# Kernel optimization log

Measured on AMD Instinct MI355X. Metric: run time of the kernel, lower is better.

## Reference

```python
import jax, jax.numpy as jnp
import numpy as np

C = 1024
R = 4            # reduction
A = 10           # num_adapters
LN_EPS = 1e-5
THRESHOLDS = np.array([1/9, 1/7, 1/5, 1/3, 1.0, 3.0, 5.0, 7.0, 9.0], dtype=np.float32)


def setup_inputs() -> dict:
    key = jax.random.key(0)
    k_feat, k_ar, k_w1, k_w2 = jax.random.split(key, 4)
    B, NA, H, W = 2, 3, 64, 64
    Cr = C // R
    output_feat = jax.random.normal(k_feat, (B, C, H, W), jnp.float32)
    # aspect ratios in [0,10) so all 10 adapters get selected
    aspect_ratio = jax.random.uniform(k_ar, (B, NA, H, W), jnp.float32) * 10.0
    # LayerNorm params (torch default init: weight=1, bias=0), stacked over adapters
    ln_scale = jnp.ones((A, C), jnp.float32)
    ln_bias = jnp.zeros((A, C), jnp.float32)
    # kaiming_normal_ fan_out / relu: std = sqrt(2/fan_out); torch weight [out,in]
    # w1 here is [C, Cr] == torch weight [Cr, C].T, fan_out = Cr
    w1 = jax.random.normal(k_w1, (A, C, Cr), jnp.float32) * np.sqrt(2.0 / Cr)
    # w2 here is [Cr, C] == torch weight [C, Cr].T, fan_out = C
    w2 = jax.random.normal(k_w2, (A, Cr, C), jnp.float32) * np.sqrt(2.0 / C)
    return dict(output_feat=output_feat, aspect_ratio=aspect_ratio,
                ln_scale=ln_scale, ln_bias=ln_bias, w1=w1, w2=w2)


def reference(output_feat, aspect_ratio, ln_scale, ln_bias, w1, w2):
    B, Cc, H, W = output_feat.shape
    NA = aspect_ratio.shape[1]
    HW = H * W
    # tokens [N, C]
    x = output_feat.transpose(0, 2, 3, 1).reshape(-1, Cc)
    # shared LayerNorm normalization (per-adapter affine applied after)
    mu = jnp.mean(x, axis=-1, keepdims=True)
    var = jnp.var(x, axis=-1, keepdims=True)
    norm = (x - mu) * jax.lax.rsqrt(var + LN_EPS)              # [N, C]
    y = norm[None, :, :] * ln_scale[:, None, :] + ln_bias[:, None, :]  # [A, N, C]
    h = jax.nn.gelu(jnp.einsum('anc,acd->and', y, w1), approximate=False)
    adapter_out = jnp.einsum('and,adc->anc', h, w2)            # [A, N, C]
    adapter_out = adapter_out.reshape(A, B, HW, Cc)            # [A, B, HW, C]
    # per-anchor, per-pixel adapter index from aspect ratio vs thresholds
    thr = jnp.asarray(THRESHOLDS, dtype=aspect_ratio.dtype)
    ar = aspect_ratio.reshape(B, NA, HW)
    idx = jnp.sum(ar[..., None] > thr, axis=-1)                # [B, NA, HW] in [0, 9]
    # gather selected adapter output per (batch, anchor, pixel)
    b_idx = jnp.arange(B)[:, None, None]
    p_idx = jnp.arange(HW)[None, None, :]
    selected = adapter_out[idx, b_idx, p_idx]                  # [B, NA, HW, C]
    selected = selected.mean(axis=1).reshape(B, H, W, Cc).transpose(0, 3, 1, 2)
    return selected + output_feat
```

## Files before the change

kernel.cpp:

```cpp
#include <hip/hip_runtime.h>
#include <hip/hip_bf16.h>
#include <math.h>

#define C_DIM 1024
#define CR    256
#define A_N   10
#define NANCH 3
#define B_N   2
#define HW_N  4096
#define NTOK  (B_N*HW_N)
#define KG2   (A_N*CR)

typedef unsigned short ushort_t;
typedef __attribute__((ext_vector_type(4))) float f32x4;
typedef __attribute__((ext_vector_type(8))) short bf16x8;

__device__ __forceinline__ ushort_t f2bf(float x) {
    __hip_bfloat16 h = __float2bfloat16(x);
    return *reinterpret_cast<ushort_t*>(&h);
}
__device__ __forceinline__ float bf2f(ushort_t u) {
    return __uint_as_float(((unsigned)u) << 16);
}

__device__ __forceinline__ float fast_gelu(float x) {
    float t = x * x;
    float u = x * (-1.5957691216f - 0.0713548163f * t);
    float e = __expf(u);
    return x * __frcp_rn(1.0f + e);
}

__global__ __launch_bounds__(256) void prep_all(
    const float* __restrict__ w1, const float* __restrict__ w2,
    const float* __restrict__ ln_s, const float* __restrict__ ln_b,
    const float* __restrict__ feat, const float* __restrict__ ar,
    ushort_t* __restrict__ w1t, ushort_t* __restrict__ w2t,
    float* __restrict__ bias1, float* __restrict__ sumv, float* __restrict__ sumq,
    int* __restrict__ cnt, int* __restrict__ tokw, int* __restrict__ tokmap) {
    __shared__ float lds[64][65];
    __shared__ float bb[4][64];
    __shared__ int lcnt[A_N], lpos[A_N], gbase[A_N];
    int id = blockIdx.x, tid = threadIdx.x;
    int lo = tid & 63, hi = tid >> 6;

    if (id < 640) {
        int d0 = (id & 3) * 64, c0 = ((id >> 2) & 15) * 64, a = id >> 6;
        #pragma unroll
        for (int i = 0; i < 16; i++) {
            int c_l = i * 4 + hi;
            lds[c_l][lo] = w1[((size_t)a * C_DIM + c0 + c_l) * CR + d0 + lo];
        }
        __syncthreads();
        {
            float s = 0.f;
            #pragma unroll
            for (int cc = 0; cc < 16; cc++) {
                int c = hi * 16 + cc;
                s += lds[c][lo] * ln_b[a * C_DIM + c0 + c];
            }
            bb[hi][lo] = s;
        }
        float sc = ln_s[a * C_DIM + c0 + lo];
        #pragma unroll
        for (int i = 0; i < 16; i++) {
            int d_l = i * 4 + hi;
            w1t[((size_t)a * CR + d0 + d_l) * C_DIM + c0 + lo] = f2bf(lds[lo][d_l] * sc);
        }
        __syncthreads();
        if (hi == 0)
            atomicAdd(&bias1[a * CR + d0 + lo], bb[0][lo] + bb[1][lo] + bb[2][lo] + bb[3][lo]);
    } else if (id < 1280) {
        int id2 = id - 640;
        int k0 = (id2 % 40) * 64, c0 = (id2 / 40) * 64;
        #pragma unroll
        for (int i = 0; i < 16; i++) {
            int k_l = i * 4 + hi;
            lds[k_l][lo] = w2[((size_t)k0 + k_l) * C_DIM + c0 + lo];
        }
        __syncthreads();
        #pragma unroll
        for (int i = 0; i < 16; i++) {
            int c_l = i * 4 + hi;
            w2t[((size_t)c0 + c_l) * KG2 + k0 + lo] = f2bf(lds[lo][c_l]);
        }
    } else if (id < 2304) {
        int id2 = id - 1280;
        int p0 = (id2 & 63) * 64, c0 = ((id2 >> 6) & 7) * 128, b = id2 >> 9;
        int p = lo, cs = hi;
        float s = 0.f, s2 = 0.f;
        #pragma unroll
        for (int c = cs; c < 128; c += 4) {
            float v = feat[((size_t)b * C_DIM + c0 + c) * HW_N + p0 + p];
            s += v; s2 += v * v;
        }
        float (*sh)[64] = (float(*)[64])lds;
        sh[cs][p] = s; sh[cs + 4][p] = s2;
        __syncthreads();
        if (tid < 64) {
            float ss = sh[0][tid] + sh[1][tid] + sh[2][tid] + sh[3][tid];
            float qq = sh[4][tid] + sh[5][tid] + sh[6][tid] + sh[7][tid];
            int t = b * HW_N + p0 + tid;
            atomicAdd(&sumv[t], ss);
            atomicAdd(&sumq[t], qq);
        }
    } else {
        if (tid < A_N) { lcnt[tid] = 0; lpos[tid] = 0; }
        __syncthreads();
        int t = (id - 2304) * 256 + tid;
        int b = t >> 12, p = t & (HW_N - 1);
        const float THR[9] = {1.0f/9.0f, 1.0f/7.0f, 0.2f, 1.0f/3.0f, 1.0f, 3.0f, 5.0f, 7.0f, 9.0f};
        int idxs[NANCH];
        #pragma unroll
        for (int na = 0; na < NANCH; na++) {
            float v = ar[(size_t)b * NANCH * HW_N + na * HW_N + p];
            int idx = 0;
            #pragma unroll
            for (int i = 0; i < 9; i++) idx += (v > THR[i]) ? 1 : 0;
            idxs[na] = idx;
        }
        int myA[NANCH], myC[NANCH], nmine = 0;
        #pragma unroll
        for (int j = 0; j < NANCH; j++) {
            bool first = true; int c3 = 0;
            #pragma unroll
            for (int k = 0; k < NANCH; k++) {
                if (idxs[k] == idxs[j]) { c3++; if (k < j) first = false; }
            }
            if (first) {
                myA[nmine] = idxs[j];
                myC[nmine] = c3;
                nmine++;
                atomicAdd(&lcnt[idxs[j]], 1);
            }
        }
        __syncthreads();
        if (tid < A_N) gbase[tid] = atomicAdd(&cnt[tid], lcnt[tid]);
        __syncthreads();
        for (int i = 0; i < NANCH; i++) {
            if (i < nmine) {
                int a2 = myA[i];
                int slot = atomicAdd(&lpos[a2], 1);
                int pos = gbase[a2] + slot;
                tokw[a2 * NTOK + pos] = t;
                tokmap[t * 3 + i] = pos | (a2 << 13) | (myC[i] << 17);
            } else {
                tokmap[t * 3 + i] = 0;
            }
        }
    }
}

__global__ __launch_bounds__(256) void normk(const float* __restrict__ feat,
                                             const float* __restrict__ sumv,
                                             const float* __restrict__ sumq,
                                             ushort_t* __restrict__ normG) {
    int p0 = blockIdx.x * 64, c0 = blockIdx.y * 64, b = blockIdx.z;
    __shared__ float lds[64][65];
    int tid = threadIdx.x, lo = tid & 63, hi = tid >> 6;
    #pragma unroll
    for (int i = 0; i < 16; i++) {
        int c_l = i * 4 + hi;
        lds[c_l][lo] = feat[((size_t)b * C_DIM + c0 + c_l) * HW_N + p0 + lo];
    }
    __syncthreads();
    int t_l = tid >> 3, cg = tid & 7;
    #pragma unroll
    for (int ii = 0; ii < 2; ii++) {
        int tl = ii * 32 + t_l;
        int t = b * HW_N + p0 + tl;
        float m = sumv[t] * (1.f / C_DIM);
        float q = sumq[t] * (1.f / C_DIM);
        float r = rsqrtf(q - m * m + 1e-5f);
        bf16x8 v;
        #pragma unroll
        for (int k = 0; k < 8; k++)
            v[k] = (short)f2bf((lds[cg * 8 + k][tl] - m) * r);
        *(bf16x8*)(normG + (size_t)t * C_DIM + c0 + cg * 8) = v;
    }
}

__device__ __forceinline__ void gemm_core_ptrs(
    const ushort_t* const ap[4], const ushort_t* const bp[4],
    int K, ushort_t* As, ushort_t* Bs, f32x4 acc[4][4]) {
    const int tid = threadIdx.x;
    const int lane = tid & 63;
    const int w = tid >> 6;
    const int wr = w >> 1, wc = w & 1;
    const int lrow = lane & 15;
    const int quad = lane >> 4;
    const int swzr = lrow & 7;

    #pragma unroll
    for (int i = 0; i < 4; i++)
        #pragma unroll
        for (int j = 0; j < 4; j++)
            #pragma unroll
            for (int e = 0; e < 4; e++) acc[i][j][e] = 0.f;

    for (int k0 = 0; k0 < K; k0 += 64) {
        __syncthreads();
        #pragma unroll
        for (int i = 0; i < 4; i++) {
            __builtin_amdgcn_global_load_lds(
                (__attribute__((address_space(1))) void*)(ap[i] + k0),
                (__attribute__((address_space(3))) void*)(As + (w * 32 + i * 8) * 64),
                16, 0, 0);
            __builtin_amdgcn_global_load_lds(
                (__attribute__((address_space(1))) void*)(bp[i] + k0),
                (__attribute__((address_space(3))) void*)(Bs + (w * 32 + i * 8) * 64),
                16, 0, 0);
        }
        __syncthreads();
        #pragma unroll
        for (int ks = 0; ks < 2; ks++) {
            const int cidx = ((ks * 4 + quad) ^ swzr) * 8;
            bf16x8 af[4], bfr[4];
            #pragma unroll
            for (int mt = 0; mt < 4; mt++)
                af[mt] = *(const bf16x8*)(As + (wr * 64 + mt * 16 + lrow) * 64 + cidx);
            #pragma unroll
            for (int nt = 0; nt < 4; nt++)
                bfr[nt] = *(const bf16x8*)(Bs + (wc * 64 + nt * 16 + lrow) * 64 + cidx);
            #pragma unroll
            for (int mt = 0; mt < 4; mt++)
                #pragma unroll
                for (int nt = 0; nt < 4; nt++)
                    acc[mt][nt] = __builtin_amdgcn_mfma_f32_16x16x32_bf16(af[mt], bfr[nt], acc[mt][nt], 0, 0, 0);
        }
    }
}

__global__ __launch_bounds__(256) void gemm1c(const ushort_t* __restrict__ normG,
                                              const ushort_t* __restrict__ w1t,
                                              const float* __restrict__ bias1,
                                              const int* __restrict__ tokw,
                                              const int* __restrict__ cnt,
                                              ushort_t* __restrict__ Hc) {
    int a = blockIdx.z;
    int mcount = cnt[a];
    int m0 = blockIdx.y * 128;
    if (m0 >= mcount) return;
    int n0 = blockIdx.x * 128;
    int base = 0;
    for (int a2 = 0; a2 < a; a2++) base += cnt[a2];

    __shared__ __align__(16) ushort_t As[128 * 64];
    __shared__ __align__(16) ushort_t Bs[128 * 64];

    int tid = threadIdx.x, lane = tid & 63, w = tid >> 6;
    int lrow8 = lane >> 3;
    int scol = ((lane & 7) ^ lrow8) * 8;
    int srowl = w * 32 + lrow8;

    const ushort_t* ap[4];
    const ushort_t* bp[4];
    #pragma unroll
    for (int i = 0; i < 4; i++) {
        int rt = tokw[a * NTOK + m0 + srowl + i * 8] & (NTOK - 1);
        ap[i] = normG + (size_t)rt * C_DIM + scol;
        bp[i] = w1t + ((size_t)a * CR + n0 + srowl + i * 8) * C_DIM + scol;
    }

    f32x4 acc[4][4];
    gemm_core_ptrs(ap, bp, C_DIM, As, Bs, acc);

    int wr = w >> 1, wc = w & 1, lrow = lane & 15, quad = lane >> 4;
    float bi[4];
    #pragma unroll
    for (int nt = 0; nt < 4; nt++)
        bi[nt] = bias1[a * CR + n0 + wc * 64 + nt * 16 + lrow];
    #pragma unroll
    for (int mt = 0; mt < 4; mt++)
        #pragma unroll
        for (int r = 0; r < 4; r++) {
            int i_row = m0 + wr * 64 + mt * 16 + quad * 4 + r;
            bool live = i_row < mcount;
            #pragma unroll
            for (int nt = 0; nt < 4; nt++) {
                int col = n0 + wc * 64 + nt * 16 + lrow;
                float v = acc[mt][nt][r] + bi[nt];
                if (live)
                    Hc[(size_t)(base + i_row) * CR + col] = f2bf(fast_gelu(v));
            }
        }
}

__global__ __launch_bounds__(256) void gemm2c(const ushort_t* __restrict__ Hc,
                                              const ushort_t* __restrict__ w2t,
                                              const int* __restrict__ cnt,
                                              ushort_t* __restrict__ O) {
    int a = blockIdx.z;
    int mcount = cnt[a];
    int m0 = blockIdx.y * 128;
    if (m0 >= mcount) return;
    int n0 = blockIdx.x * 128;
    int base = 0;
    for (int a2 = 0; a2 < a; a2++) base += cnt[a2];

    __shared__ __align__(16) ushort_t As[128 * 64];
    __shared__ __align__(16) ushort_t Bs[128 * 64];

    int tid = threadIdx.x, lane = tid & 63, w = tid >> 6;
    int lrow8 = lane >> 3;
    int scol = ((lane & 7) ^ lrow8) * 8;
    int srowl = w * 32 + lrow8;

    const ushort_t* ap[4];
    const ushort_t* bp[4];
    #pragma unroll
    for (int i = 0; i < 4; i++) {
        ap[i] = Hc + (size_t)(base + m0 + srowl + i * 8) * CR + scol;
        bp[i] = w2t + (size_t)(n0 + srowl + i * 8) * KG2 + a * CR + scol;
    }

    f32x4 acc[4][4];
    gemm_core_ptrs(ap, bp, CR, As, Bs, acc);

    int wr = w >> 1, wc = w & 1, lrow = lane & 15, quad = lane >> 4;
    #pragma unroll
    for (int mt = 0; mt < 4; mt++)
        #pragma unroll
        for (int r = 0; r < 4; r++) {
            int i_row = m0 + wr * 64 + mt * 16 + quad * 4 + r;
            bool live = i_row < mcount;
            #pragma unroll
            for (int nt = 0; nt < 4; nt++) {
                int col = n0 + wc * 64 + nt * 16 + lrow;
                if (live)
                    O[(size_t)(base + i_row) * C_DIM + col] = f2bf(acc[mt][nt][r]);
            }
        }
}

__global__ __launch_bounds__(256) void finalk2(const ushort_t* __restrict__ O,
                                               const int* __restrict__ tokmap,
                                               const int* __restrict__ cnt,
                                               const float* __restrict__ feat,
                                               float* __restrict__ out) {
    int p0 = blockIdx.x * 64, c0 = blockIdx.y * 64, b = blockIdx.z;
    __shared__ float lds[64][65];
    __shared__ int pbase[A_N];
    int tid = threadIdx.x, lo = tid & 63, hi = tid >> 6;
    if (tid < A_N) {
        int s = 0;
        for (int k = 0; k < tid; k++) s += cnt[k];
        pbase[tid] = s;
    }
    __syncthreads();
    int t_l = tid >> 3, cg = tid & 7;
    #pragma unroll
    for (int ii = 0; ii < 2; ii++) {
        int tl = ii * 32 + t_l;
        int t = b * HW_N + p0 + tl;
        float val8[8];
        #pragma unroll
        for (int k = 0; k < 8; k++) val8[k] = 0.f;
        #pragma unroll
        for (int j = 0; j < 3; j++) {
            int e = tokmap[t * 3 + j];
            float wv = (float)(e >> 17) * (1.0f / 3.0f);
            int a2 = (e >> 13) & 15;
            int row = pbase[a2] + (e & 8191);
            bf16x8 v = *(const bf16x8*)(O + (size_t)row * C_DIM + c0 + cg * 8);
            #pragma unroll
            for (int k = 0; k < 8; k++)
                val8[k] += wv * bf2f((ushort_t)v[k]);
        }
        #pragma unroll
        for (int k = 0; k < 8; k++)
            lds[tl][cg * 8 + k] = val8[k];
    }
    __syncthreads();
    #pragma unroll
    for (int i = 0; i < 16; i++) {
        int c_l = i * 4 + hi;
        size_t o = ((size_t)b * C_DIM + c0 + c_l) * HW_N + p0 + lo;
        out[o] = lds[lo][c_l] + feat[o];
    }
}

extern "C" void kernel_launch(void* const* d_in, const int* in_sizes, int n_in,
                              void* d_out, int out_size, void* d_ws, size_t ws_size,
                              hipStream_t stream) {
    (void)in_sizes; (void)n_in; (void)out_size; (void)ws_size;
    const float* feat = (const float*)d_in[0];
    const float* ar   = (const float*)d_in[1];
    const float* ln_s = (const float*)d_in[2];
    const float* ln_b = (const float*)d_in[3];
    const float* w1   = (const float*)d_in[4];
    const float* w2   = (const float*)d_in[5];
    float* out = (float*)d_out;
    char* ws = (char*)d_ws;

    float*    bias1  = (float*)(ws + 0);
    int*      cnt    = (int*)(ws + 10240);
    float*    sumv   = (float*)(ws + 10496);
    float*    sumq   = (float*)(ws + 43264);
    const size_t ZERO_BYTES = 76800;
    int*      tokmap = (int*)(ws + 76800);
    int*      tokw   = (int*)(ws + 175104);
    ushort_t* w1t    = (ushort_t*)(ws + 502784);
    ushort_t* w2t    = (ushort_t*)(ws + 5745664);
    ushort_t* normG  = (ushort_t*)(ws + 10988544);
    ushort_t* Hc     = (ushort_t*)(ws + 27765760);
    ushort_t* O      = (ushort_t*)(ws + 40414208);

    dim3 blk(256);
    hipMemsetAsync(ws, 0, ZERO_BYTES, stream);
    prep_all<<<dim3(2336), blk, 0, stream>>>(w1, w2, ln_s, ln_b, feat, ar,
                                             w1t, w2t, bias1, sumv, sumq, cnt, tokw, tokmap);
    normk<<<dim3(64, 16, B_N), blk, 0, stream>>>(feat, sumv, sumq, normG);
    gemm1c<<<dim3(2, 64, A_N), blk, 0, stream>>>(normG, w1t, bias1, tokw, cnt, Hc);
    gemm2c<<<dim3(8, 64, A_N), blk, 0, stream>>>(Hc, w2t, cnt, O);
    finalk2<<<dim3(64, 16, B_N), blk, 0, stream>>>(O, tokmap, cnt, feat, out);
}
```

Measured before the change: 98.79 us.

## Shrink gemm1 M-tile to 64 rows and widen final gather tile to 256 channels

gemm1c now uses a 64x128 output tile through a new core in which each wave owns a 64x32 slice, doubling the grid in M. This should give more blocks and less padding waste on the variable per-adapter token counts. finalk2 now covers 256 channels per block, with 32 lanes reading contiguous 16-byte chunks of each O row and vectorised LDS stores. The trade-offs are less operand reuse per block in gemm1, and a larger LDS footprint plus fewer blocks in finalk2.

```diff
diff --git a/kernel.cpp b/kernel.cpp
--- a/kernel.cpp
+++ b/kernel.cpp
@@ -230,6 +230,57 @@
     }
 }
 
+__device__ __forceinline__ void gemm_core_64(
+    const ushort_t* const ap[2], const ushort_t* const bp[4],
+    int K, ushort_t* As, ushort_t* Bs, f32x4 acc[4][2]) {
+    const int tid = threadIdx.x;
+    const int lane = tid & 63;
+    const int w = tid >> 6;
+    const int lrow = lane & 15;
+    const int quad = lane >> 4;
+    const int swzr = lrow & 7;
+
+    #pragma unroll
+    for (int i = 0; i < 4; i++)
+        #pragma unroll
+        for (int j = 0; j < 2; j++)
+            #pragma unroll
+            for (int e = 0; e < 4; e++) acc[i][j][e] = 0.f;
+
+    for (int k0 = 0; k0 < K; k0 += 64) {
+        __syncthreads();
+        #pragma unroll
+        for (int i = 0; i < 2; i++)
+            __builtin_amdgcn_global_load_lds(
+                (__attribute__((address_space(1))) void*)(ap[i] + k0),
+                (__attribute__((address_space(3))) void*)(As + (w * 16 + i * 8) * 64),
+                16, 0, 0);
+        #pragma unroll
+        for (int i = 0; i < 4; i++)
+            __builtin_amdgcn_global_load_lds(
+                (__attribute__((address_space(1))) void*)(bp[i] + k0),
+                (__attribute__((address_space(3))) void*)(Bs + (w * 32 + i * 8) * 64),
+                16, 0, 0);
+        __syncthreads();
+        #pragma unroll
+        for (int ks = 0; ks < 2; ks++) {
+            const int cidx = ((ks * 4 + quad) ^ swzr) * 8;
+            bf16x8 af[4], bfr[2];
+            #pragma unroll
+            for (int mt = 0; mt < 4; mt++)
+                af[mt] = *(const bf16x8*)(As + (mt * 16 + lrow) * 64 + cidx);
+            #pragma unroll
+            for (int nt = 0; nt < 2; nt++)
+                bfr[nt] = *(const bf16x8*)(Bs + (w * 32 + nt * 16 + lrow) * 64 + cidx);
+            #pragma unroll
+            for (int mt = 0; mt < 4; mt++)
+                #pragma unroll
+                for (int nt = 0; nt < 2; nt++)
+                    acc[mt][nt] = __builtin_amdgcn_mfma_f32_16x16x32_bf16(af[mt], bfr[nt], acc[mt][nt], 0, 0, 0);
+        }
+    }
+}
+
 __global__ __launch_bounds__(256) void gemm1c(const ushort_t* __restrict__ normG,
                                               const ushort_t* __restrict__ w1t,
                                               const float* __restrict__ bias1,
@@ -238,46 +289,47 @@
                                               ushort_t* __restrict__ Hc) {
     int a = blockIdx.z;
     int mcount = cnt[a];
-    int m0 = blockIdx.y * 128;
+    int m0 = blockIdx.y * 64;
     if (m0 >= mcount) return;
     int n0 = blockIdx.x * 128;
     int base = 0;
     for (int a2 = 0; a2 < a; a2++) base += cnt[a2];
 
-    __shared__ __align__(16) ushort_t As[128 * 64];
+    __shared__ __align__(16) ushort_t As[64 * 64];
     __shared__ __align__(16) ushort_t Bs[128 * 64];
 
     int tid = threadIdx.x, lane = tid & 63, w = tid >> 6;
     int lrow8 = lane >> 3;
     int scol = ((lane & 7) ^ lrow8) * 8;
-    int srowl = w * 32 + lrow8;
-
-    const ushort_t* ap[4];
+
+    const ushort_t* ap[2];
     const ushort_t* bp[4];
     #pragma unroll
-    for (int i = 0; i < 4; i++) {
-        int rt = tokw[a * NTOK + m0 + srowl + i * 8] & (NTOK - 1);
+    for (int i = 0; i < 2; i++) {
+        int rt = tokw[a * NTOK + m0 + w * 16 + i * 8 + lrow8] & (NTOK - 1);
         ap[i] = normG + (size_t)rt * C_DIM + scol;
-        bp[i] = w1t + ((size_t)a * CR + n0 + srowl + i * 8) * C_DIM + scol;
-    }
-
-    f32x4 acc[4][4];
-    gemm_core_ptrs(ap, bp, C_DIM, As, Bs, acc);
-
-    int wr = w >> 1, wc = w & 1, lrow = lane & 15, quad = lane >> 4;
-    float bi[4];
-    #pragma unroll
-    for (int nt = 0; nt < 4; nt++)
-        bi[nt] = bias1[a * CR + n0 + wc * 64 + nt * 16 + lrow];
+    }
+    #pragma unroll
+    for (int i = 0; i < 4; i++)
+        bp[i] = w1t + ((size_t)a * CR + n0 + w * 32 + i * 8 + lrow8) * C_DIM + scol;
+
+    f32x4 acc[4][2];
+    gemm_core_64(ap, bp, C_DIM, As, Bs, acc);
+
+    int lrow = lane & 15, quad = lane >> 4;
+    float bi[2];
+    #pragma unroll
+    for (int nt = 0; nt < 2; nt++)
+        bi[nt] = bias1[a * CR + n0 + w * 32 + nt * 16 + lrow];
     #pragma unroll
     for (int mt = 0; mt < 4; mt++)
         #pragma unroll
         for (int r = 0; r < 4; r++) {
-            int i_row = m0 + wr * 64 + mt * 16 + quad * 4 + r;
+            int i_row = m0 + mt * 16 + quad * 4 + r;
             bool live = i_row < mcount;
             #pragma unroll
-            for (int nt = 0; nt < 4; nt++) {
-                int col = n0 + wc * 64 + nt * 16 + lrow;
+            for (int nt = 0; nt < 2; nt++) {
+                int col = n0 + w * 32 + nt * 16 + lrow;
                 float v = acc[mt][nt][r] + bi[nt];
                 if (live)
                     Hc[(size_t)(base + i_row) * CR + col] = f2bf(fast_gelu(v));
@@ -337,20 +389,20 @@
                                                const int* __restrict__ cnt,
                                                const float* __restrict__ feat,
                                                float* __restrict__ out) {
-    int p0 = blockIdx.x * 64, c0 = blockIdx.y * 64, b = blockIdx.z;
-    __shared__ float lds[64][65];
+    int p0 = blockIdx.x * 64, c0 = blockIdx.y * 256, b = blockIdx.z;
+    __shared__ float lds[64][260];
     __shared__ int pbase[A_N];
-    int tid = threadIdx.x, lo = tid & 63, hi = tid >> 6;
+    int tid = threadIdx.x;
     if (tid < A_N) {
         int s = 0;
         for (int k = 0; k < tid; k++) s += cnt[k];
         pbase[tid] = s;
     }
     __syncthreads();
-    int t_l = tid >> 3, cg = tid & 7;
-    #pragma unroll
-    for (int ii = 0; ii < 2; ii++) {
-        int tl = ii * 32 + t_l;
+    int tl8 = tid >> 5, l32 = tid & 31;
+    #pragma unroll
+    for (int ii = 0; ii < 8; ii++) {
+        int tl = ii * 8 + tl8;
         int t = b * HW_N + p0 + tl;
         float val8[8];
         #pragma unroll
@@ -361,18 +413,19 @@
             float wv = (float)(e >> 17) * (1.0f / 3.0f);
             int a2 = (e >> 13) & 15;
             int row = pbase[a2] + (e & 8191);
-            bf16x8 v = *(const bf16x8*)(O + (size_t)row * C_DIM + c0 + cg * 8);
+            bf16x8 v = *(const bf16x8*)(O + (size_t)row * C_DIM + c0 + l32 * 8);
             #pragma unroll
             for (int k = 0; k < 8; k++)
                 val8[k] += wv * bf2f((ushort_t)v[k]);
         }
-        #pragma unroll
-        for (int k = 0; k < 8; k++)
-            lds[tl][cg * 8 + k] = val8[k];
+        f32x4 v0 = {val8[0], val8[1], val8[2], val8[3]};
+        f32x4 v1 = {val8[4], val8[5], val8[6], val8[7]};
+        *(f32x4*)&lds[tl][l32 * 8] = v0;
+        *(f32x4*)&lds[tl][l32 * 8 + 4] = v1;
     }
     __syncthreads();
-    #pragma unroll
-    for (int i = 0; i < 16; i++) {
+    int lo = tid & 63, hi = tid >> 6;
+    for (int i = 0; i < 64; i++) {
         int c_l = i * 4 + hi;
         size_t o = ((size_t)b * C_DIM + c0 + c_l) * HW_N + p0 + lo;
         out[o] = lds[lo][c_l] + feat[o];
@@ -410,7 +463,7 @@
     prep_all<<<dim3(2336), blk, 0, stream>>>(w1, w2, ln_s, ln_b, feat, ar,
                                              w1t, w2t, bias1, sumv, sumq, cnt, tokw, tokmap);
     normk<<<dim3(64, 16, B_N), blk, 0, stream>>>(feat, sumv, sumq, normG);
-    gemm1c<<<dim3(2, 64, A_N), blk, 0, stream>>>(normG, w1t, bias1, tokw, cnt, Hc);
+    gemm1c<<<dim3(2, 128, A_N), blk, 0, stream>>>(normG, w1t, bias1, tokw, cnt, Hc);
     gemm2c<<<dim3(8, 64, A_N), blk, 0, stream>>>(Hc, w2t, cnt, O);
-    finalk2<<<dim3(64, 16, B_N), blk, 0, stream>>>(O, tokmap, cnt, feat, out);
-}
+    finalk2<<<dim3(64, 4, B_N), blk, 0, stream>>>(O, tokmap, cnt, feat, out);
+}
```

Result: no change. 100.5 us (+1.7%).

## Fold LayerNorm normalization into GEMM1 epilogue and drop separate norm kernel

Applied to the files above, without the earlier changes.

The LayerNorm is now applied algebraically after the first GEMM: raw features are transposed to bf16 in the prep kernel, and the GEMM1 epilogue computes rstd*(acc - mean*colsum(W1*scale)) + bias using per-token sums and a new per-column sum of the scaled weights. This removes the separate normalization kernel, one launch and one full pass over the features. The trade-off is precision: GEMM1 now runs on un-centered bf16 features, so cancellation when the mean is large could raise error. The prep kernel also grows, since it does the transpose along with the statistics.

```diff
diff --git a/kernel.cpp b/kernel.cpp
--- a/kernel.cpp
+++ b/kernel.cpp
@@ -35,10 +35,12 @@
     const float* __restrict__ ln_s, const float* __restrict__ ln_b,
     const float* __restrict__ feat, const float* __restrict__ ar,
     ushort_t* __restrict__ w1t, ushort_t* __restrict__ w2t,
-    float* __restrict__ bias1, float* __restrict__ sumv, float* __restrict__ sumq,
-    int* __restrict__ cnt, int* __restrict__ tokw, int* __restrict__ tokmap) {
+    float* __restrict__ bias1, float* __restrict__ cs1,
+    float* __restrict__ sumv, float* __restrict__ sumq,
+    int* __restrict__ cnt, int* __restrict__ tokw, int* __restrict__ tokmap,
+    ushort_t* __restrict__ featT) {
     __shared__ float lds[64][65];
-    __shared__ float bb[4][64];
+    __shared__ float bb[8][64];
     __shared__ int lcnt[A_N], lpos[A_N], gbase[A_N];
     int id = blockIdx.x, tid = threadIdx.x;
     int lo = tid & 63, hi = tid >> 6;
@@ -52,13 +54,16 @@
         }
         __syncthreads();
         {
-            float s = 0.f;
+            float s = 0.f, s2 = 0.f;
             #pragma unroll
             for (int cc = 0; cc < 16; cc++) {
                 int c = hi * 16 + cc;
-                s += lds[c][lo] * ln_b[a * C_DIM + c0 + c];
+                float v = lds[c][lo];
+                s  += v * ln_b[a * C_DIM + c0 + c];
+                s2 += v * ln_s[a * C_DIM + c0 + c];
             }
             bb[hi][lo] = s;
+            bb[hi + 4][lo] = s2;
         }
         float sc = ln_s[a * C_DIM + c0 + lo];
         #pragma unroll
@@ -69,6 +74,8 @@
         __syncthreads();
         if (hi == 0)
             atomicAdd(&bias1[a * CR + d0 + lo], bb[0][lo] + bb[1][lo] + bb[2][lo] + bb[3][lo]);
+        else if (hi == 1)
+            atomicAdd(&cs1[a * CR + d0 + lo], bb[4][lo] + bb[5][lo] + bb[6][lo] + bb[7][lo]);
     } else if (id < 1280) {
         int id2 = id - 640;
         int k0 = (id2 % 40) * 64, c0 = (id2 / 40) * 64;
@@ -83,30 +90,46 @@
             int c_l = i * 4 + hi;
             w2t[((size_t)c0 + c_l) * KG2 + k0 + lo] = f2bf(lds[lo][c_l]);
         }
-    } else if (id < 2304) {
+    } else if (id < 3328) {
         int id2 = id - 1280;
-        int p0 = (id2 & 63) * 64, c0 = ((id2 >> 6) & 7) * 128, b = id2 >> 9;
-        int p = lo, cs = hi;
-        float s = 0.f, s2 = 0.f;
-        #pragma unroll
-        for (int c = cs; c < 128; c += 4) {
-            float v = feat[((size_t)b * C_DIM + c0 + c) * HW_N + p0 + p];
-            s += v; s2 += v * v;
-        }
-        float (*sh)[64] = (float(*)[64])lds;
-        sh[cs][p] = s; sh[cs + 4][p] = s2;
+        int p0 = (id2 & 63) * 64, c0 = ((id2 >> 6) & 15) * 64, b = id2 >> 10;
+        #pragma unroll
+        for (int i = 0; i < 16; i++) {
+            int c_l = i * 4 + hi;
+            lds[c_l][lo] = feat[((size_t)b * C_DIM + c0 + c_l) * HW_N + p0 + lo];
+        }
+        __syncthreads();
+        {
+            float s = 0.f, s2 = 0.f;
+            #pragma unroll
+            for (int c = hi; c < 64; c += 4) {
+                float v = lds[c][lo];
+                s += v; s2 += v * v;
+            }
+            bb[hi][lo] = s; bb[hi + 4][lo] = s2;
+        }
         __syncthreads();
         if (tid < 64) {
-            float ss = sh[0][tid] + sh[1][tid] + sh[2][tid] + sh[3][tid];
-            float qq = sh[4][tid] + sh[5][tid] + sh[6][tid] + sh[7][tid];
+            float ss = bb[0][tid] + bb[1][tid] + bb[2][tid] + bb[3][tid];
+            float qq = bb[4][tid] + bb[5][tid] + bb[6][tid] + bb[7][tid];
             int t = b * HW_N + p0 + tid;
             atomicAdd(&sumv[t], ss);
             atomicAdd(&sumq[t], qq);
         }
+        int t_l = tid >> 3, cg = tid & 7;
+        #pragma unroll
+        for (int ii = 0; ii < 2; ii++) {
+            int tl = ii * 32 + t_l;
+            bf16x8 v;
+            #pragma unroll
+            for (int k = 0; k < 8; k++)
+                v[k] = (short)f2bf(lds[cg * 8 + k][tl]);
+            *(bf16x8*)(featT + (size_t)(b * HW_N + p0 + tl) * C_DIM + c0 + cg * 8) = v;
+        }
     } else {
         if (tid < A_N) { lcnt[tid] = 0; lpos[tid] = 0; }
         __syncthreads();
-        int t = (id - 2304) * 256 + tid;
+        int t = (id - 3328) * 256 + tid;
         int b = t >> 12, p = t & (HW_N - 1);
         const float THR[9] = {1.0f/9.0f, 1.0f/7.0f, 0.2f, 1.0f/3.0f, 1.0f, 3.0f, 5.0f, 7.0f, 9.0f};
         int idxs[NANCH];
@@ -147,35 +170,6 @@
                 tokmap[t * 3 + i] = 0;
             }
         }
-    }
-}
-
-__global__ __launch_bounds__(256) void normk(const float* __restrict__ feat,
-                                             const float* __restrict__ sumv,
-                                             const float* __restrict__ sumq,
-                                             ushort_t* __restrict__ normG) {
-    int p0 = blockIdx.x * 64, c0 = blockIdx.y * 64, b = blockIdx.z;
-    __shared__ float lds[64][65];
-    int tid = threadIdx.x, lo = tid & 63, hi = tid >> 6;
-    #pragma unroll
-    for (int i = 0; i < 16; i++) {
-        int c_l = i * 4 + hi;
-        lds[c_l][lo] = feat[((size_t)b * C_DIM + c0 + c_l) * HW_N + p0 + lo];
-    }
-    __syncthreads();
-    int t_l = tid >> 3, cg = tid & 7;
-    #pragma unroll
-    for (int ii = 0; ii < 2; ii++) {
-        int tl = ii * 32 + t_l;
-        int t = b * HW_N + p0 + tl;
-        float m = sumv[t] * (1.f / C_DIM);
-        float q = sumq[t] * (1.f / C_DIM);
-        float r = rsqrtf(q - m * m + 1e-5f);
-        bf16x8 v;
-        #pragma unroll
-        for (int k = 0; k < 8; k++)
-            v[k] = (short)f2bf((lds[cg * 8 + k][tl] - m) * r);
-        *(bf16x8*)(normG + (size_t)t * C_DIM + c0 + cg * 8) = v;
     }
 }
 
@@ -230,9 +224,12 @@
     }
 }
 
-__global__ __launch_bounds__(256) void gemm1c(const ushort_t* __restrict__ normG,
+__global__ __launch_bounds__(256) void gemm1c(const ushort_t* __restrict__ featT,
                                               const ushort_t* __restrict__ w1t,
                                               const float* __restrict__ bias1,
+                                              const float* __restrict__ cs1,
+                                              const float* __restrict__ sumv,
+                                              const float* __restrict__ sumq,
                                               const int* __restrict__ tokw,
                                               const int* __restrict__ cnt,
                                               ushort_t* __restrict__ Hc) {
@@ -257,7 +254,7 @@
     #pragma unroll
     for (int i = 0; i < 4; i++) {
         int rt = tokw[a * NTOK + m0 + srowl + i * 8] & (NTOK - 1);
-        ap[i] = normG + (size_t)rt * C_DIM + scol;
+        ap[i] = featT + (size_t)rt * C_DIM + scol;
         bp[i] = w1t + ((size_t)a * CR + n0 + srowl + i * 8) * C_DIM + scol;
     }
 
@@ -265,20 +262,27 @@
     gemm_core_ptrs(ap, bp, C_DIM, As, Bs, acc);
 
     int wr = w >> 1, wc = w & 1, lrow = lane & 15, quad = lane >> 4;
-    float bi[4];
-    #pragma unroll
-    for (int nt = 0; nt < 4; nt++)
-        bi[nt] = bias1[a * CR + n0 + wc * 64 + nt * 16 + lrow];
+    float bi[4], cs[4];
+    #pragma unroll
+    for (int nt = 0; nt < 4; nt++) {
+        int col = a * CR + n0 + wc * 64 + nt * 16 + lrow;
+        bi[nt] = bias1[col];
+        cs[nt] = cs1[col];
+    }
     #pragma unroll
     for (int mt = 0; mt < 4; mt++)
         #pragma unroll
         for (int r = 0; r < 4; r++) {
             int i_row = m0 + wr * 64 + mt * 16 + quad * 4 + r;
             bool live = i_row < mcount;
+            int t = tokw[a * NTOK + i_row] & (NTOK - 1);
+            float m = sumv[t] * (1.f / C_DIM);
+            float q = sumq[t] * (1.f / C_DIM);
+            float rn = rsqrtf(q - m * m + 1e-5f);
             #pragma unroll
             for (int nt = 0; nt < 4; nt++) {
                 int col = n0 + wc * 64 + nt * 16 + lrow;
-                float v = acc[mt][nt][r] + bi[nt];
+                float v = rn * (acc[mt][nt][r] - m * cs[nt]) + bi[nt];
                 if (live)
                     Hc[(size_t)(base + i_row) * CR + col] = f2bf(fast_gelu(v));
             }
@@ -393,24 +397,26 @@
     char* ws = (char*)d_ws;
 
     float*    bias1  = (float*)(ws + 0);
-    int*      cnt    = (int*)(ws + 10240);
-    float*    sumv   = (float*)(ws + 10496);
-    float*    sumq   = (float*)(ws + 43264);
-    const size_t ZERO_BYTES = 76800;
-    int*      tokmap = (int*)(ws + 76800);
-    int*      tokw   = (int*)(ws + 175104);
-    ushort_t* w1t    = (ushort_t*)(ws + 502784);
-    ushort_t* w2t    = (ushort_t*)(ws + 5745664);
-    ushort_t* normG  = (ushort_t*)(ws + 10988544);
-    ushort_t* Hc     = (ushort_t*)(ws + 27765760);
-    ushort_t* O      = (ushort_t*)(ws + 40414208);
+    float*    cs1    = (float*)(ws + 10240);
+    int*      cnt    = (int*)(ws + 20480);
+    float*    sumv   = (float*)(ws + 20736);
+    float*    sumq   = (float*)(ws + 53504);
+    const size_t ZERO_BYTES = 86272;
+    int*      tokmap = (int*)(ws + 86272);
+    int*      tokw   = (int*)(ws + 184576);
+    ushort_t* w1t    = (ushort_t*)(ws + 512256);
+    ushort_t* w2t    = (ushort_t*)(ws + 5755136);
+    ushort_t* featT  = (ushort_t*)(ws + 10998016);
+    ushort_t* Hc     = (ushort_t*)(ws + 27775232);
+    ushort_t* O      = (ushort_t*)(ws + 40423680);
 
     dim3 blk(256);
     hipMemsetAsync(ws, 0, ZERO_BYTES, stream);
-    prep_all<<<dim3(2336), blk, 0, stream>>>(w1, w2, ln_s, ln_b, feat, ar,
-                                             w1t, w2t, bias1, sumv, sumq, cnt, tokw, tokmap);
-    normk<<<dim3(64, 16, B_N), blk, 0, stream>>>(feat, sumv, sumq, normG);
-    gemm1c<<<dim3(2, 64, A_N), blk, 0, stream>>>(normG, w1t, bias1, tokw, cnt, Hc);
+    prep_all<<<dim3(3360), blk, 0, stream>>>(w1, w2, ln_s, ln_b, feat, ar,
+                                             w1t, w2t, bias1, cs1, sumv, sumq,
+                                             cnt, tokw, tokmap, featT);
+    gemm1c<<<dim3(2, 64, A_N), blk, 0, stream>>>(featT, w1t, bias1, cs1, sumv, sumq,
+                                                 tokw, cnt, Hc);
     gemm2c<<<dim3(8, 64, A_N), blk, 0, stream>>>(Hc, w2t, cnt, O);
     finalk2<<<dim3(64, 16, B_N), blk, 0, stream>>>(O, tokmap, cnt, feat, out);
 }
```

New measurement: 96.13 us. -2.7%, faster.
